# Kernel tuning notes

Hardware: AMD Instinct MI355X
Metric: run time of the kernel (lower is better)

Reference implementation:

```python
import jax, jax.numpy as jnp
import numpy as np

DIM = 256
NUM_HEADS = 8
HEAD_DIM = DIM // NUM_HEADS          # 32
KEY_DIM = int(HEAD_DIM * 0.5)        # 16
SCALE = KEY_DIM ** (-0.5)
QKV_OUT = DIM + 2 * KEY_DIM * NUM_HEADS  # 512
BN_EPS = 1e-3


def _bn(x, gamma, beta, mean, var):
    # inference-mode BatchNorm2d over channel axis 1 of NCHW
    inv = gamma / jnp.sqrt(var + BN_EPS)
    return x * inv[None, :, None, None] + (beta - mean * inv)[None, :, None, None]


def _conv1x1(x, w):
    # w: (O, C, 1, 1)
    return jnp.einsum('bchw,oc->bohw', x, w[:, :, 0, 0])


def _dwconv3x3(x, w):
    # depthwise 3x3, SAME padding; w: (C, 1, 3, 3)
    return jax.lax.conv_general_dilated(
        x, w, window_strides=(1, 1), padding='SAME',
        feature_group_count=x.shape[1],
        dimension_numbers=('NCHW', 'OIHW', 'NCHW'))


def setup_inputs() -> dict:
    key = jax.random.key(0)
    ks = jax.random.split(key, 16)
    B, C, H, W = 16, DIM, 32, 32
    inp = {
        'x': jax.random.normal(ks[0], (B, C, H, W), jnp.float32),
        'qkv_w': jax.random.normal(ks[1], (QKV_OUT, DIM, 1, 1), jnp.float32) * (1.0 / np.sqrt(DIM)),
        'qkv_gamma': jnp.ones((QKV_OUT,), jnp.float32),
        'qkv_beta': jnp.zeros((QKV_OUT,), jnp.float32),
        'qkv_mean': jax.random.normal(ks[2], (QKV_OUT,), jnp.float32) * 0.1,
        'qkv_var': jax.random.uniform(ks[3], (QKV_OUT,), jnp.float32, 0.5, 1.5),
        'pe_w': jax.random.normal(ks[4], (DIM, 1, 3, 3), jnp.float32) * (1.0 / 3.0),
        'pe_gamma': jnp.ones((DIM,), jnp.float32),
        'pe_beta': jnp.zeros((DIM,), jnp.float32),
        'pe_mean': jax.random.normal(ks[5], (DIM,), jnp.float32) * 0.1,
        'pe_var': jax.random.uniform(ks[6], (DIM,), jnp.float32, 0.5, 1.5),
        'proj_w': jax.random.normal(ks[7], (DIM, DIM, 1, 1), jnp.float32) * (1.0 / np.sqrt(DIM)),
        'proj_gamma': jnp.ones((DIM,), jnp.float32),
        'proj_beta': jnp.zeros((DIM,), jnp.float32),
        'proj_mean': jax.random.normal(ks[8], (DIM,), jnp.float32) * 0.1,
        'proj_var': jax.random.uniform(ks[9], (DIM,), jnp.float32, 0.5, 1.5),
    }
    return inp


def reference(x, qkv_w, qkv_gamma, qkv_beta, qkv_mean, qkv_var,
              pe_w, pe_gamma, pe_beta, pe_mean, pe_var,
              proj_w, proj_gamma, proj_beta, proj_mean, proj_var):
    B, C, H, W = x.shape
    N = H * W
    # qkv: 1x1 conv + BN (act=False)
    qkv = _bn(_conv1x1(x, qkv_w), qkv_gamma, qkv_beta, qkv_mean, qkv_var)
    qkv = qkv.reshape(B, NUM_HEADS, 2 * KEY_DIM + HEAD_DIM, N)
    q = qkv[:, :, :KEY_DIM]                          # (B, h, kd, N)
    k = qkv[:, :, KEY_DIM:2 * KEY_DIM]               # (B, h, kd, N)
    v = qkv[:, :, 2 * KEY_DIM:]                      # (B, h, hd, N)
    # attn = (q^T @ k) * scale, softmax over last dim
    attn = jnp.einsum('bhdn,bhdm->bhnm', q, k) * SCALE   # (B, h, N, N)
    attn = jax.nn.softmax(attn, axis=-1)
    # v @ attn^T
    v_attn = jnp.einsum('bhdn,bhmn->bhdm', v, attn)      # (B, h, hd, N)
    v_attn = v_attn.reshape(B, C, H, W)
    v_reshaped = v.reshape(B, C, H, W)
    pos_enc = _bn(_dwconv3x3(v_reshaped, pe_w), pe_gamma, pe_beta, pe_mean, pe_var)
    out = v_attn + pos_enc
    out = _bn(_conv1x1(out, proj_w), proj_gamma, proj_beta, proj_mean, proj_var)
    return out
```

## Files before the change

kernel.cpp:

```cpp
#include <hip/hip_runtime.h>

#define B_ 16
#define C_ 256
#define N_ 1024
#define NH 8
#define HD 32
#define KD 16
#define QKV_OUT_ 512
#define BN_EPS 1e-3f
#define SCALE2_ (0.25f * 1.44269504088896f)

typedef __attribute__((ext_vector_type(8))) short short8;
typedef __attribute__((ext_vector_type(16))) float float16;

__device__ inline unsigned short f2bf(float f) {
  unsigned int u = __float_as_uint(f);
  return (unsigned short)((u + 0x7FFF + ((u >> 16) & 1)) >> 16);
}
__device__ inline float bf2f(unsigned short s) {
  return __uint_as_float(((unsigned int)s) << 16);
}
__device__ inline float16 zero16() {
  float16 z;
  #pragma unroll
  for (int i = 0; i < 16; ++i) z[i] = 0.f;
  return z;
}
__device__ inline unsigned int pack_bf16_trunc(float a, float b) {
  return __builtin_amdgcn_perm(__float_as_uint(b), __float_as_uint(a), 0x07060302u);
}
__device__ inline unsigned int pack_bf16_rne(float a, float b) {
  return (unsigned int)f2bf(a) | ((unsigned int)f2bf(b) << 16);
}
__device__ inline float fast_exp2(float x) {
#if __has_builtin(__builtin_amdgcn_exp2f)
  return __builtin_amdgcn_exp2f(x);
#else
  return exp2f(x);
#endif
}
__device__ inline void pl32(unsigned int& a, unsigned int& b) {
#if __has_builtin(__builtin_amdgcn_permlane32_swap)
  typedef __attribute__((ext_vector_type(2))) int int2v;
  int2v r = __builtin_amdgcn_permlane32_swap((int)a, (int)b, false, false);
  a = (unsigned int)r[0];
  b = (unsigned int)r[1];
#else
  unsigned int ea = (unsigned int)__shfl_xor((int)a, 32, 64);
  unsigned int eb = (unsigned int)__shfl_xor((int)b, 32, 64);
  bool hi = (threadIdx.x & 32) != 0;
  unsigned int an = hi ? eb : a;
  unsigned int bn = hi ? b : ea;
  a = an; b = bn;
#endif
}
__device__ inline short8 lds_frag(const unsigned short* p) {
  union { uint2 u[2]; short8 s; } r;
  r.u[0] = *(const uint2*)p;
  r.u[1] = *(const uint2*)(p + 4);
  return r.s;
}
__device__ inline void lds_store16(unsigned short* p, uint4 v) {
  *(uint2*)p = make_uint2(v.x, v.y);
  *(uint2*)(p + 4) = make_uint2(v.z, v.w);
}

__global__ __launch_bounds__(256) void fold_weights(
    const float* __restrict__ qkv_w, const float* __restrict__ qg,
    const float* __restrict__ qb, const float* __restrict__ qm,
    const float* __restrict__ qv,
    const float* __restrict__ proj_w, const float* __restrict__ pg,
    const float* __restrict__ pb, const float* __restrict__ pm,
    const float* __restrict__ pv,
    unsigned short* __restrict__ wq, float* __restrict__ biasq,
    unsigned short* __restrict__ wp, float* __restrict__ biasp)
{
  const int o = blockIdx.x, c = threadIdx.x;
  if (o < QKV_OUT_) {
    float s = ((o & 63) < 16) ? SCALE2_ : 1.f;
    float inv = qg[o] * rsqrtf(qv[o] + BN_EPS) * s;
    wq[o * C_ + c] = f2bf(qkv_w[o * C_ + c] * inv);
    if (c == 0) biasq[o] = qb[o] * s - qm[o] * inv;
  } else {
    int oo = o - QKV_OUT_;
    float inv = pg[oo] * rsqrtf(pv[oo] + BN_EPS);
    wp[oo * C_ + c] = f2bf(proj_w[oo * C_ + c] * inv);
    if (c == 0) biasp[oo] = pb[oo] - pm[oo] * inv;
  }
}

__global__ __launch_bounds__(256) void transpose_x(
    const float* __restrict__ x, unsigned short* __restrict__ xT)
{
  __shared__ float t[64][69];
  const int tid = threadIdx.x;
  const int nt = blockIdx.x, ct = blockIdx.y, b = blockIdx.z;
  const int n0 = nt * 64, c0 = ct * 64;

  #pragma unroll
  for (int it = 0; it < 4; ++it) {
    int cl = it * 16 + (tid >> 4);
    int nl = (tid & 15) * 4;
    float4 v = *(const float4*)(x + ((size_t)b * C_ + c0 + cl) * N_ + n0 + nl);
    t[cl][nl + 0] = v.x; t[cl][nl + 1] = v.y;
    t[cl][nl + 2] = v.z; t[cl][nl + 3] = v.w;
  }
  __syncthreads();

  const int nr = tid >> 2, cseg = (tid & 3) * 16;
  unsigned int pk[8];
  #pragma unroll
  for (int q = 0; q < 8; ++q)
    pk[q] = pack_bf16_rne(t[cseg + 2 * q][nr], t[cseg + 2 * q + 1][nr]);
  unsigned short* row = xT + ((size_t)b * N_ + n0 + nr) * C_ + c0 + cseg;
  *(uint4*)(row)     = make_uint4(pk[0], pk[1], pk[2], pk[3]);
  *(uint4*)(row + 8) = make_uint4(pk[4], pk[5], pk[6], pk[7]);
}

template <int MODE>
__global__ __launch_bounds__(256) void gemm_tiled(
    const unsigned short* __restrict__ inT, const unsigned short* __restrict__ wfold,
    const float* __restrict__ bias,
    unsigned short* __restrict__ qkT, unsigned short* __restrict__ vbuf,
    float* __restrict__ outf)
{
  constexpr int STR = 44;
  __shared__ __align__(8) unsigned short wa[2][128 * STR];
  __shared__ __align__(8) unsigned short xb[2][128 * STR];
  const int tid = threadIdx.x;
  const int wave = tid >> 6, lane = tid & 63, l31 = lane & 31, lh = lane >> 5;
  const int wm = wave & 1, wn = wave >> 1;
  const int n0g = blockIdx.x * 128;
  const int o0 = blockIdx.y * 128;
  const int b = n0g >> 10, nloc = n0g & 1023;

  const int r0 = tid >> 2, oc0 = (tid & 3) * 8;
  const int r1 = (tid + 256) >> 2, oc1 = oc0;

  float16 acc[2][2];
  #pragma unroll
  for (int i = 0; i < 2; ++i)
    #pragma unroll
    for (int j = 0; j < 2; ++j) acc[i][j] = zero16();

  uint4 ga0, ga1, gb0, gb1;
  #define LOADK(kc)                                                          \
    ga0 = *(const uint4*)(wfold + (size_t)(o0 + r0) * C_ + (kc) * 32 + oc0); \
    ga1 = *(const uint4*)(wfold + (size_t)(o0 + r1) * C_ + (kc) * 32 + oc1); \
    gb0 = *(const uint4*)(inT + (size_t)(n0g + r0) * C_ + (kc) * 32 + oc0);  \
    gb1 = *(const uint4*)(inT + (size_t)(n0g + r1) * C_ + (kc) * 32 + oc1);
  #define STOREK(bufi)                                   \
    lds_store16(&wa[bufi][r0 * STR + oc0], ga0);         \
    lds_store16(&wa[bufi][r1 * STR + oc1], ga1);         \
    lds_store16(&xb[bufi][r0 * STR + oc0], gb0);         \
    lds_store16(&xb[bufi][r1 * STR + oc1], gb1);

  LOADK(0);
  STOREK(0);
  __syncthreads();

  for (int kc = 0; kc < 8; ++kc) {
    const int buf = kc & 1;
    if (kc < 7) { LOADK(kc + 1); }

    #pragma unroll
    for (int ks = 0; ks < 2; ++ks) {
      const int ko = ks * 16 + lh * 8;
      short8 a0 = lds_frag(&wa[buf][(wm * 64 + l31) * STR + ko]);
      short8 a1 = lds_frag(&wa[buf][(wm * 64 + 32 + l31) * STR + ko]);
      short8 b0 = lds_frag(&xb[buf][(wn * 64 + l31) * STR + ko]);
      short8 b1 = lds_frag(&xb[buf][(wn * 64 + 32 + l31) * STR + ko]);
      acc[0][0] = __builtin_amdgcn_mfma_f32_32x32x16_bf16(a0, b0, acc[0][0], 0, 0, 0);
      acc[0][1] = __builtin_amdgcn_mfma_f32_32x32x16_bf16(a0, b1, acc[0][1], 0, 0, 0);
      acc[1][0] = __builtin_amdgcn_mfma_f32_32x32x16_bf16(a1, b0, acc[1][0], 0, 0, 0);
      acc[1][1] = __builtin_amdgcn_mfma_f32_32x32x16_bf16(a1, b1, acc[1][1], 0, 0, 0);
    }

    if (kc < 7) { STOREK(buf ^ 1); }
    __syncthreads();
  }
  #undef LOADK
  #undef STOREK

  if constexpr (MODE == 0) {
    const int hh = (o0 >> 6) + wm;
    #pragma unroll
    for (int bn = 0; bn < 2; ++bn) {
      int n = nloc + wn * 64 + bn * 32 + l31;
      unsigned short* row = qkT + (((size_t)b * NH + hh) * N_ + n) * 32;
      #pragma unroll
      for (int qd = 0; qd < 4; ++qd) {
        int cc0 = 8 * qd + 4 * lh;
        ushort4 rv;
        rv.x = f2bf(acc[0][bn][4 * qd + 0] + bias[hh * 64 + cc0 + 0]);
        rv.y = f2bf(acc[0][bn][4 * qd + 1] + bias[hh * 64 + cc0 + 1]);
        rv.z = f2bf(acc[0][bn][4 * qd + 2] + bias[hh * 64 + cc0 + 2]);
        rv.w = f2bf(acc[0][bn][4 * qd + 3] + bias[hh * 64 + cc0 + 3]);
        *(ushort4*)(row + cc0) = rv;
      }
    }
    #pragma unroll
    for (int r = 0; r < 16; ++r) {
      int d = (r & 3) + 8 * (r >> 2) + 4 * lh;
      float bo = bias[hh * 64 + 32 + d];
      unsigned short* vrow =
          vbuf + ((size_t)b * C_ + hh * 32 + d) * N_ + nloc + wn * 64 + l31;
      #pragma unroll
      for (int bn = 0; bn < 2; ++bn)
        vrow[bn * 32] = f2bf(acc[1][bn][r] + bo);
    }
  } else {
    #pragma unroll
    for (int am = 0; am < 2; ++am) {
      #pragma unroll
      for (int r = 0; r < 16; ++r) {
        int o = o0 + wm * 64 + am * 32 + (r & 3) + 8 * (r >> 2) + 4 * lh;
        float bo = bias[o];
        float* orow = outf + ((size_t)b * C_ + o) * N_ + nloc + wn * 64 + l31;
        #pragma unroll
        for (int bn = 0; bn < 2; ++bn)
          orow[bn * 32] = acc[am][bn][r] + bo;
      }
    }
  }
}

__global__ __launch_bounds__(256) void dwconv_bn(
    const unsigned short* __restrict__ vbuf, const float* __restrict__ pw,
    const float* __restrict__ gamma, const float* __restrict__ beta,
    const float* __restrict__ mean, const float* __restrict__ var,
    unsigned short* __restrict__ posb)
{
  __shared__ float t[34][34];
  const int c = blockIdx.x, b = blockIdx.y;
  const int tid = threadIdx.x;
  const unsigned short* vp = vbuf + ((size_t)b * C_ + c) * N_;

  #pragma unroll
  for (int r = 0; r < 4; ++r) {
    int idx = r * 256 + tid;
    t[(idx >> 5) + 1][(idx & 31) + 1] = bf2f(vp[idx]);
  }
  if (tid < 34) {
    t[0][tid] = 0.f; t[33][tid] = 0.f;
    t[tid][0] = 0.f; t[tid][33] = 0.f;
  }
  __syncthreads();

  float w9[9];
  #pragma unroll
  for (int i = 0; i < 9; ++i) w9[i] = pw[c * 9 + i];
  float inv = gamma[c] * rsqrtf(var[c] + BN_EPS);
  float add = beta[c] - mean[c] * inv;

  unsigned short* op = posb + ((size_t)b * C_ + c) * N_;
  #pragma unroll
  for (int r = 0; r < 4; ++r) {
    int idx = r * 256 + tid;
    int y = idx >> 5, x = idx & 31;
    float s = 0.f;
    #pragma unroll
    for (int dy = 0; dy < 3; ++dy)
      #pragma unroll
      for (int dx = 0; dx < 3; ++dx)
        s += t[y + dy][x + dx] * w9[dy * 3 + dx];
    op[idx] = f2bf(s * inv + add);
  }
}

__global__ __launch_bounds__(256) void attn_mfma(
    const unsigned short* __restrict__ qkT, const unsigned short* __restrict__ vbuf,
    const unsigned short* __restrict__ posb, unsigned short* __restrict__ vattnT)
{
  __shared__ __align__(8) unsigned short k_lds[2][128 * 28];
  __shared__ __align__(8) unsigned short v_lds[2][32 * 140];

  const int tid = threadIdx.x;
  const int wave = tid >> 6, lane = tid & 63;
  const int l31 = lane & 31, lh = lane >> 5;
  const int h = blockIdx.y, b = blockIdx.z;
  const int qbase = blockIdx.x * 256 + wave * 64;

  const unsigned short* qkb = qkT + ((size_t)b * NH + h) * N_ * 32;
  const unsigned short* vhead = vbuf + ((size_t)b * C_ + h * HD) * N_;

  const int skey = tid >> 1, shalf = tid & 1;
  const int svd = tid >> 3, svseg = tid & 7;

  short8 qfA = lds_frag(qkb + (size_t)(qbase + l31) * 32 + lh * 8);
  short8 qfB = lds_frag(qkb + (size_t)(qbase + 32 + l31) * 32 + lh * 8);

  uint4 gk, gv0, gv1;
  #define LOADC(kc)                                                             \
    gk  = *(const uint4*)(qkb + (size_t)((kc) + skey) * 32 + 16 + shalf * 8);   \
    gv0 = *(const uint4*)(vhead + (size_t)svd * N_ + (kc) + svseg * 16);        \
    gv1 = *(const uint4*)(vhead + (size_t)svd * N_ + (kc) + svseg * 16 + 8);
  #define STOREC(bufi)                                        \
    lds_store16(&k_lds[bufi][skey * 28 + shalf * 8], gk);     \
    lds_store16(&v_lds[bufi][svd * 140 + svseg * 16], gv0);   \
    lds_store16(&v_lds[bufi][svd * 140 + svseg * 16 + 8], gv1);

  LOADC(0);
  STOREC(0);
  __syncthreads();

  float16 oaccA = zero16(), oaccB = zero16();
  float lsA[4] = {0.f, 0.f, 0.f, 0.f}, lsB[4] = {0.f, 0.f, 0.f, 0.f};

  for (int c = 0; c < 8; ++c) {
    const int buf = c & 1;
    if (c < 7) { LOADC((c + 1) * 128); }

    #pragma unroll
    for (int t = 0; t < 4; ++t) {
      const int key0 = t * 32;
      short8 kf = lds_frag(&k_lds[buf][(key0 + l31) * 28 + lh * 8]);
      float16 stA = __builtin_amdgcn_mfma_f32_32x32x16_bf16(kf, qfA, zero16(), 0, 0, 0);
      float16 stB = __builtin_amdgcn_mfma_f32_32x32x16_bf16(kf, qfB, zero16(), 0, 0, 0);

      unsigned int uA[8], uB[8];
      #pragma unroll
      for (int q = 0; q < 8; ++q) {
        float pe = fast_exp2(stA[2 * q]);
        float po = fast_exp2(stA[2 * q + 1]);
        lsA[q & 3] += pe + po;
        uA[q] = pack_bf16_trunc(pe, po);
      }
      #pragma unroll
      for (int q = 0; q < 8; ++q) {
        float pe = fast_exp2(stB[2 * q]);
        float po = fast_exp2(stB[2 * q + 1]);
        lsB[q & 3] += pe + po;
        uB[q] = pack_bf16_trunc(pe, po);
      }

      #pragma unroll
      for (int f = 0; f < 2; ++f) {
        short8 vf = lds_frag(&v_lds[buf][l31 * 140 + key0 + f * 16 + lh * 8]);
        const int q0 = f * 4;
        {
          unsigned int a0 = uA[q0], a2 = uA[q0 + 2]; pl32(a0, a2);
          unsigned int a1 = uA[q0 + 1], a3 = uA[q0 + 3]; pl32(a1, a3);
          union { unsigned int w[4]; short8 s; } bf;
          bf.w[0] = a0; bf.w[1] = a1; bf.w[2] = a2; bf.w[3] = a3;
          oaccA = __builtin_amdgcn_mfma_f32_32x32x16_bf16(vf, bf.s, oaccA, 0, 0, 0);
        }
        {
          unsigned int a0 = uB[q0], a2 = uB[q0 + 2]; pl32(a0, a2);
          unsigned int a1 = uB[q0 + 1], a3 = uB[q0 + 3]; pl32(a1, a3);
          union { unsigned int w[4]; short8 s; } bf;
          bf.w[0] = a0; bf.w[1] = a1; bf.w[2] = a2; bf.w[3] = a3;
          oaccB = __builtin_amdgcn_mfma_f32_32x32x16_bf16(vf, bf.s, oaccB, 0, 0, 0);
        }
      }
    }

    if (c < 7) { STOREC(buf ^ 1); }
    __syncthreads();
  }
  #undef LOADC
  #undef STOREC

  float lsumA = (lsA[0] + lsA[1]) + (lsA[2] + lsA[3]);
  float lsumB = (lsB[0] + lsB[1]) + (lsB[2] + lsB[3]);
  lsumA += __shfl_xor(lsumA, 32, 64);
  lsumB += __shfl_xor(lsumB, 32, 64);
  const float linvA = 1.f / lsumA, linvB = 1.f / lsumB;

  #pragma unroll
  for (int g = 0; g < 2; ++g) {
    const float16& oacc = g ? oaccB : oaccA;
    const float linv = g ? linvB : linvA;
    const int token = qbase + g * 32 + l31;
    float val[16];
    #pragma unroll
    for (int r = 0; r < 16; ++r) {
      int d = (r & 3) + 8 * (r >> 2) + 4 * lh;
      val[r] = oacc[r] * linv +
               bf2f(posb[((size_t)b * C_ + h * HD + d) * N_ + token]);
    }
    unsigned int u[8];
    #pragma unroll
    for (int m = 0; m < 8; ++m) u[m] = pack_bf16_rne(val[2 * m], val[2 * m + 1]);
    pl32(u[0], u[4]); pl32(u[1], u[5]); pl32(u[2], u[6]); pl32(u[3], u[7]);
    unsigned short* row = vattnT + ((size_t)b * N_ + token) * C_ + h * HD + lh * 16;
    *(uint4*)(row)     = make_uint4(u[0], u[1], u[4], u[5]);
    *(uint4*)(row + 8) = make_uint4(u[2], u[3], u[6], u[7]);
  }
}

extern "C" void kernel_launch(void* const* d_in, const int* in_sizes, int n_in,
                              void* d_out, int out_size, void* d_ws, size_t ws_size,
                              hipStream_t stream) {
  const float* x          = (const float*)d_in[0];
  const float* qkv_w      = (const float*)d_in[1];
  const float* qkv_gamma  = (const float*)d_in[2];
  const float* qkv_beta   = (const float*)d_in[3];
  const float* qkv_mean   = (const float*)d_in[4];
  const float* qkv_var    = (const float*)d_in[5];
  const float* pe_w       = (const float*)d_in[6];
  const float* pe_gamma   = (const float*)d_in[7];
  const float* pe_beta    = (const float*)d_in[8];
  const float* pe_mean    = (const float*)d_in[9];
  const float* pe_var     = (const float*)d_in[10];
  const float* proj_w     = (const float*)d_in[11];
  const float* proj_gamma = (const float*)d_in[12];
  const float* proj_beta  = (const float*)d_in[13];
  const float* proj_mean  = (const float*)d_in[14];
  const float* proj_var   = (const float*)d_in[15];
  float* out = (float*)d_out;

  char* ws = (char*)d_ws;
  unsigned short* qkT = (unsigned short*)ws;
  ws += (size_t)B_ * NH * N_ * 32 * sizeof(unsigned short);
  unsigned short* vbuf = (unsigned short*)ws;
  ws += (size_t)B_ * C_ * N_ * sizeof(unsigned short);
  unsigned short* xT = (unsigned short*)ws;
  ws += (size_t)B_ * N_ * C_ * sizeof(unsigned short);
  unsigned short* vattnT = (unsigned short*)ws;
  ws += (size_t)B_ * N_ * C_ * sizeof(unsigned short);
  unsigned short* posb = (unsigned short*)ws;
  ws += (size_t)B_ * C_ * N_ * sizeof(unsigned short);
  unsigned short* wq = (unsigned short*)ws;
  ws += (size_t)QKV_OUT_ * C_ * sizeof(unsigned short);
  unsigned short* wp = (unsigned short*)ws;
  ws += (size_t)C_ * C_ * sizeof(unsigned short);
  float* biasq = (float*)ws; ws += QKV_OUT_ * sizeof(float);
  float* biasp = (float*)ws;

  fold_weights<<<dim3(QKV_OUT_ + C_), 256, 0, stream>>>(
      qkv_w, qkv_gamma, qkv_beta, qkv_mean, qkv_var,
      proj_w, proj_gamma, proj_beta, proj_mean, proj_var,
      wq, biasq, wp, biasp);
  transpose_x<<<dim3(16, 4, 16), 256, 0, stream>>>(x, xT);

  gemm_tiled<0><<<dim3(128, 4), 256, 0, stream>>>(
      xT, wq, biasq, qkT, vbuf, nullptr);

  dwconv_bn<<<dim3(C_, B_), 256, 0, stream>>>(
      vbuf, pe_w, pe_gamma, pe_beta, pe_mean, pe_var, posb);

  attn_mfma<<<dim3(4, NH, B_), 256, 0, stream>>>(qkT, vbuf, posb, vattnT);

  gemm_tiled<1><<<dim3(128, 2), 256, 0, stream>>>(
      vattnT, wp, biasp, nullptr, nullptr, out);
}
```

Measured before the change: 161.3 us.

## Fuse x transpose into QKV GEMM and halve attention queries per block

Drops the separate transpose_x kernel. The QKV GEMM now reads fp32 x directly in NCHW, converts it to bf16 and writes it transposed into LDS, which removes one launch and the round trip of the xT buffer through global memory. The attention kernel gives each wave 32 queries instead of 64 and uses 128 queries per block, so the grid grows from 512 to 1024 blocks for more parallelism and fewer registers per wave. The cost is that each K/V tile is loaded into LDS twice as often, and the strided per-element global loads of x in the GEMM may coalesce less well.

```diff
diff --git a/kernel.cpp b/kernel.cpp
--- a/kernel.cpp
+++ b/kernel.cpp
@@ -89,40 +89,10 @@
   }
 }
 
-__global__ __launch_bounds__(256) void transpose_x(
-    const float* __restrict__ x, unsigned short* __restrict__ xT)
-{
-  __shared__ float t[64][69];
-  const int tid = threadIdx.x;
-  const int nt = blockIdx.x, ct = blockIdx.y, b = blockIdx.z;
-  const int n0 = nt * 64, c0 = ct * 64;
-
-  #pragma unroll
-  for (int it = 0; it < 4; ++it) {
-    int cl = it * 16 + (tid >> 4);
-    int nl = (tid & 15) * 4;
-    float4 v = *(const float4*)(x + ((size_t)b * C_ + c0 + cl) * N_ + n0 + nl);
-    t[cl][nl + 0] = v.x; t[cl][nl + 1] = v.y;
-    t[cl][nl + 2] = v.z; t[cl][nl + 3] = v.w;
-  }
-  __syncthreads();
-
-  const int nr = tid >> 2, cseg = (tid & 3) * 16;
-  unsigned int pk[8];
-  #pragma unroll
-  for (int q = 0; q < 8; ++q)
-    pk[q] = pack_bf16_rne(t[cseg + 2 * q][nr], t[cseg + 2 * q + 1][nr]);
-  unsigned short* row = xT + ((size_t)b * N_ + n0 + nr) * C_ + c0 + cseg;
-  *(uint4*)(row)     = make_uint4(pk[0], pk[1], pk[2], pk[3]);
-  *(uint4*)(row + 8) = make_uint4(pk[4], pk[5], pk[6], pk[7]);
-}
-
-template <int MODE>
-__global__ __launch_bounds__(256) void gemm_tiled(
-    const unsigned short* __restrict__ inT, const unsigned short* __restrict__ wfold,
+__global__ __launch_bounds__(256) void gemm_qkv(
+    const float* __restrict__ x, const unsigned short* __restrict__ wq,
     const float* __restrict__ bias,
-    unsigned short* __restrict__ qkT, unsigned short* __restrict__ vbuf,
-    float* __restrict__ outf)
+    unsigned short* __restrict__ qkT, unsigned short* __restrict__ vbuf)
 {
   constexpr int STR = 44;
   __shared__ __align__(8) unsigned short wa[2][128 * STR];
@@ -130,12 +100,33 @@
   const int tid = threadIdx.x;
   const int wave = tid >> 6, lane = tid & 63, l31 = lane & 31, lh = lane >> 5;
   const int wm = wave & 1, wn = wave >> 1;
-  const int n0g = blockIdx.x * 128;
+  const int b = blockIdx.x >> 3, nloc = (blockIdx.x & 7) * 128;
   const int o0 = blockIdx.y * 128;
-  const int b = n0g >> 10, nloc = n0g & 1023;
 
   const int r0 = tid >> 2, oc0 = (tid & 3) * 8;
-  const int r1 = (tid + 256) >> 2, oc1 = oc0;
+  const int r1 = r0 + 64;
+  const int tok = tid & 127, chalf = (tid >> 7) * 16;
+  const float* xbase = x + (size_t)b * C_ * N_ + nloc + tok;
+
+  uint4 ga0, ga1;
+  float nb[16];
+
+  auto loadk = [&](int kc) {
+    ga0 = *(const uint4*)(wq + (size_t)(o0 + r0) * C_ + kc * 32 + oc0);
+    ga1 = *(const uint4*)(wq + (size_t)(o0 + r1) * C_ + kc * 32 + oc0);
+    #pragma unroll
+    for (int j = 0; j < 16; ++j)
+      nb[j] = xbase[(size_t)(kc * 32 + chalf + j) * N_];
+  };
+  auto storek = [&](int bufi) {
+    lds_store16(&wa[bufi][r0 * STR + oc0], ga0);
+    lds_store16(&wa[bufi][r1 * STR + oc0], ga1);
+    unsigned int pk[8];
+    #pragma unroll
+    for (int q = 0; q < 8; ++q) pk[q] = pack_bf16_rne(nb[2 * q], nb[2 * q + 1]);
+    lds_store16(&xb[bufi][tok * STR + chalf], make_uint4(pk[0], pk[1], pk[2], pk[3]));
+    lds_store16(&xb[bufi][tok * STR + chalf + 8], make_uint4(pk[4], pk[5], pk[6], pk[7]));
+  };
 
   float16 acc[2][2];
   #pragma unroll
@@ -143,25 +134,13 @@
     #pragma unroll
     for (int j = 0; j < 2; ++j) acc[i][j] = zero16();
 
-  uint4 ga0, ga1, gb0, gb1;
-  #define LOADK(kc)                                                          \
-    ga0 = *(const uint4*)(wfold + (size_t)(o0 + r0) * C_ + (kc) * 32 + oc0); \
-    ga1 = *(const uint4*)(wfold + (size_t)(o0 + r1) * C_ + (kc) * 32 + oc1); \
-    gb0 = *(const uint4*)(inT + (size_t)(n0g + r0) * C_ + (kc) * 32 + oc0);  \
-    gb1 = *(const uint4*)(inT + (size_t)(n0g + r1) * C_ + (kc) * 32 + oc1);
-  #define STOREK(bufi)                                   \
-    lds_store16(&wa[bufi][r0 * STR + oc0], ga0);         \
-    lds_store16(&wa[bufi][r1 * STR + oc1], ga1);         \
-    lds_store16(&xb[bufi][r0 * STR + oc0], gb0);         \
-    lds_store16(&xb[bufi][r1 * STR + oc1], gb1);
-
-  LOADK(0);
-  STOREK(0);
+  loadk(0);
+  storek(0);
   __syncthreads();
 
   for (int kc = 0; kc < 8; ++kc) {
     const int buf = kc & 1;
-    if (kc < 7) { LOADK(kc + 1); }
+    if (kc < 7) loadk(kc + 1);
 
     #pragma unroll
     for (int ks = 0; ks < 2; ++ks) {
@@ -176,51 +155,110 @@
       acc[1][1] = __builtin_amdgcn_mfma_f32_32x32x16_bf16(a1, b1, acc[1][1], 0, 0, 0);
     }
 
-    if (kc < 7) { STOREK(buf ^ 1); }
+    if (kc < 7) storek(buf ^ 1);
     __syncthreads();
   }
-  #undef LOADK
-  #undef STOREK
-
-  if constexpr (MODE == 0) {
-    const int hh = (o0 >> 6) + wm;
-    #pragma unroll
-    for (int bn = 0; bn < 2; ++bn) {
-      int n = nloc + wn * 64 + bn * 32 + l31;
-      unsigned short* row = qkT + (((size_t)b * NH + hh) * N_ + n) * 32;
-      #pragma unroll
-      for (int qd = 0; qd < 4; ++qd) {
-        int cc0 = 8 * qd + 4 * lh;
-        ushort4 rv;
-        rv.x = f2bf(acc[0][bn][4 * qd + 0] + bias[hh * 64 + cc0 + 0]);
-        rv.y = f2bf(acc[0][bn][4 * qd + 1] + bias[hh * 64 + cc0 + 1]);
-        rv.z = f2bf(acc[0][bn][4 * qd + 2] + bias[hh * 64 + cc0 + 2]);
-        rv.w = f2bf(acc[0][bn][4 * qd + 3] + bias[hh * 64 + cc0 + 3]);
-        *(ushort4*)(row + cc0) = rv;
-      }
+
+  const int hh = (o0 >> 6) + wm;
+  #pragma unroll
+  for (int bn = 0; bn < 2; ++bn) {
+    int n = nloc + wn * 64 + bn * 32 + l31;
+    unsigned short* row = qkT + (((size_t)b * NH + hh) * N_ + n) * 32;
+    #pragma unroll
+    for (int qd = 0; qd < 4; ++qd) {
+      int cc0 = 8 * qd + 4 * lh;
+      ushort4 rv;
+      rv.x = f2bf(acc[0][bn][4 * qd + 0] + bias[hh * 64 + cc0 + 0]);
+      rv.y = f2bf(acc[0][bn][4 * qd + 1] + bias[hh * 64 + cc0 + 1]);
+      rv.z = f2bf(acc[0][bn][4 * qd + 2] + bias[hh * 64 + cc0 + 2]);
+      rv.w = f2bf(acc[0][bn][4 * qd + 3] + bias[hh * 64 + cc0 + 3]);
+      *(ushort4*)(row + cc0) = rv;
     }
+  }
+  #pragma unroll
+  for (int r = 0; r < 16; ++r) {
+    int d = (r & 3) + 8 * (r >> 2) + 4 * lh;
+    float bo = bias[hh * 64 + 32 + d];
+    unsigned short* vrow =
+        vbuf + ((size_t)b * C_ + hh * 32 + d) * N_ + nloc + wn * 64 + l31;
+    #pragma unroll
+    for (int bn = 0; bn < 2; ++bn)
+      vrow[bn * 32] = f2bf(acc[1][bn][r] + bo);
+  }
+}
+
+__global__ __launch_bounds__(256) void gemm_proj(
+    const unsigned short* __restrict__ inT, const unsigned short* __restrict__ wfold,
+    const float* __restrict__ bias, float* __restrict__ outf)
+{
+  constexpr int STR = 44;
+  __shared__ __align__(8) unsigned short wa[2][128 * STR];
+  __shared__ __align__(8) unsigned short xb[2][128 * STR];
+  const int tid = threadIdx.x;
+  const int wave = tid >> 6, lane = tid & 63, l31 = lane & 31, lh = lane >> 5;
+  const int wm = wave & 1, wn = wave >> 1;
+  const int n0g = blockIdx.x * 128;
+  const int o0 = blockIdx.y * 128;
+  const int b = n0g >> 10, nloc = n0g & 1023;
+
+  const int r0 = tid >> 2, oc0 = (tid & 3) * 8;
+  const int r1 = r0 + 64;
+
+  float16 acc[2][2];
+  #pragma unroll
+  for (int i = 0; i < 2; ++i)
+    #pragma unroll
+    for (int j = 0; j < 2; ++j) acc[i][j] = zero16();
+
+  uint4 ga0, ga1, gb0, gb1;
+  auto loadk = [&](int kc) {
+    ga0 = *(const uint4*)(wfold + (size_t)(o0 + r0) * C_ + kc * 32 + oc0);
+    ga1 = *(const uint4*)(wfold + (size_t)(o0 + r1) * C_ + kc * 32 + oc0);
+    gb0 = *(const uint4*)(inT + (size_t)(n0g + r0) * C_ + kc * 32 + oc0);
+    gb1 = *(const uint4*)(inT + (size_t)(n0g + r1) * C_ + kc * 32 + oc0);
+  };
+  auto storek = [&](int bufi) {
+    lds_store16(&wa[bufi][r0 * STR + oc0], ga0);
+    lds_store16(&wa[bufi][r1 * STR + oc0], ga1);
+    lds_store16(&xb[bufi][r0 * STR + oc0], gb0);
+    lds_store16(&xb[bufi][r1 * STR + oc0], gb1);
+  };
+
+  loadk(0);
+  storek(0);
+  __syncthreads();
+
+  for (int kc = 0; kc < 8; ++kc) {
+    const int buf = kc & 1;
+    if (kc < 7) loadk(kc + 1);
+
+    #pragma unroll
+    for (int ks = 0; ks < 2; ++ks) {
+      const int ko = ks * 16 + lh * 8;
+      short8 a0 = lds_frag(&wa[buf][(wm * 64 + l31) * STR + ko]);
+      short8 a1 = lds_frag(&wa[buf][(wm * 64 + 32 + l31) * STR + ko]);
+      short8 b0 = lds_frag(&xb[buf][(wn * 64 + l31) * STR + ko]);
+      short8 b1 = lds_frag(&xb[buf][(wn * 64 + 32 + l31) * STR + ko]);
+      acc[0][0] = __builtin_amdgcn_mfma_f32_32x32x16_bf16(a0, b0, acc[0][0], 0, 0, 0);
+      acc[0][1] = __builtin_amdgcn_mfma_f32_32x32x16_bf16(a0, b1, acc[0][1], 0, 0, 0);
+      acc[1][0] = __builtin_amdgcn_mfma_f32_32x32x16_bf16(a1, b0, acc[1][0], 0, 0, 0);
+      acc[1][1] = __builtin_amdgcn_mfma_f32_32x32x16_bf16(a1, b1, acc[1][1], 0, 0, 0);
+    }
+
+    if (kc < 7) storek(buf ^ 1);
+    __syncthreads();
+  }
+
+  #pragma unroll
+  for (int am = 0; am < 2; ++am) {
     #pragma unroll
     for (int r = 0; r < 16; ++r) {
-      int d = (r & 3) + 8 * (r >> 2) + 4 * lh;
-      float bo = bias[hh * 64 + 32 + d];
-      unsigned short* vrow =
-          vbuf + ((size_t)b * C_ + hh * 32 + d) * N_ + nloc + wn * 64 + l31;
+      int o = o0 + wm * 64 + am * 32 + (r & 3) + 8 * (r >> 2) + 4 * lh;
+      float bo = bias[o];
+      float* orow = outf + ((size_t)b * C_ + o) * N_ + nloc + wn * 64 + l31;
       #pragma unroll
       for (int bn = 0; bn < 2; ++bn)
-        vrow[bn * 32] = f2bf(acc[1][bn][r] + bo);
-    }
-  } else {
-    #pragma unroll
-    for (int am = 0; am < 2; ++am) {
-      #pragma unroll
-      for (int r = 0; r < 16; ++r) {
-        int o = o0 + wm * 64 + am * 32 + (r & 3) + 8 * (r >> 2) + 4 * lh;
-        float bo = bias[o];
-        float* orow = outf + ((size_t)b * C_ + o) * N_ + nloc + wn * 64 + l31;
-        #pragma unroll
-        for (int bn = 0; bn < 2; ++bn)
-          orow[bn * 32] = acc[am][bn][r] + bo;
-      }
+        orow[bn * 32] = acc[am][bn][r] + bo;
     }
   }
 }
@@ -278,8 +316,8 @@
   const int tid = threadIdx.x;
   const int wave = tid >> 6, lane = tid & 63;
   const int l31 = lane & 31, lh = lane >> 5;
-  const int h = blockIdx.y, b = blockIdx.z;
-  const int qbase = blockIdx.x * 256 + wave * 64;
+  const int b = blockIdx.x >> 3, h = blockIdx.x & 7;
+  const int qbase = blockIdx.y * 128 + wave * 32;
 
   const unsigned short* qkb = qkT + ((size_t)b * NH + h) * N_ * 32;
   const unsigned short* vhead = vbuf + ((size_t)b * C_ + h * HD) * N_;
@@ -287,106 +325,81 @@
   const int skey = tid >> 1, shalf = tid & 1;
   const int svd = tid >> 3, svseg = tid & 7;
 
-  short8 qfA = lds_frag(qkb + (size_t)(qbase + l31) * 32 + lh * 8);
-  short8 qfB = lds_frag(qkb + (size_t)(qbase + 32 + l31) * 32 + lh * 8);
+  short8 qf = lds_frag(qkb + (size_t)(qbase + l31) * 32 + lh * 8);
 
   uint4 gk, gv0, gv1;
-  #define LOADC(kc)                                                             \
-    gk  = *(const uint4*)(qkb + (size_t)((kc) + skey) * 32 + 16 + shalf * 8);   \
-    gv0 = *(const uint4*)(vhead + (size_t)svd * N_ + (kc) + svseg * 16);        \
-    gv1 = *(const uint4*)(vhead + (size_t)svd * N_ + (kc) + svseg * 16 + 8);
-  #define STOREC(bufi)                                        \
-    lds_store16(&k_lds[bufi][skey * 28 + shalf * 8], gk);     \
-    lds_store16(&v_lds[bufi][svd * 140 + svseg * 16], gv0);   \
+  auto loadc = [&](int kc) {
+    gk  = *(const uint4*)(qkb + (size_t)(kc + skey) * 32 + 16 + shalf * 8);
+    gv0 = *(const uint4*)(vhead + (size_t)svd * N_ + kc + svseg * 16);
+    gv1 = *(const uint4*)(vhead + (size_t)svd * N_ + kc + svseg * 16 + 8);
+  };
+  auto storec = [&](int bufi) {
+    lds_store16(&k_lds[bufi][skey * 28 + shalf * 8], gk);
+    lds_store16(&v_lds[bufi][svd * 140 + svseg * 16], gv0);
     lds_store16(&v_lds[bufi][svd * 140 + svseg * 16 + 8], gv1);
-
-  LOADC(0);
-  STOREC(0);
+  };
+
+  loadc(0);
+  storec(0);
   __syncthreads();
 
-  float16 oaccA = zero16(), oaccB = zero16();
-  float lsA[4] = {0.f, 0.f, 0.f, 0.f}, lsB[4] = {0.f, 0.f, 0.f, 0.f};
+  float16 oacc = zero16();
+  float ls[4] = {0.f, 0.f, 0.f, 0.f};
 
   for (int c = 0; c < 8; ++c) {
     const int buf = c & 1;
-    if (c < 7) { LOADC((c + 1) * 128); }
+    if (c < 7) loadc((c + 1) * 128);
 
     #pragma unroll
     for (int t = 0; t < 4; ++t) {
       const int key0 = t * 32;
       short8 kf = lds_frag(&k_lds[buf][(key0 + l31) * 28 + lh * 8]);
-      float16 stA = __builtin_amdgcn_mfma_f32_32x32x16_bf16(kf, qfA, zero16(), 0, 0, 0);
-      float16 stB = __builtin_amdgcn_mfma_f32_32x32x16_bf16(kf, qfB, zero16(), 0, 0, 0);
-
-      unsigned int uA[8], uB[8];
+      float16 st = __builtin_amdgcn_mfma_f32_32x32x16_bf16(kf, qf, zero16(), 0, 0, 0);
+
+      unsigned int u[8];
       #pragma unroll
       for (int q = 0; q < 8; ++q) {
-        float pe = fast_exp2(stA[2 * q]);
-        float po = fast_exp2(stA[2 * q + 1]);
-        lsA[q & 3] += pe + po;
-        uA[q] = pack_bf16_trunc(pe, po);
-      }
-      #pragma unroll
-      for (int q = 0; q < 8; ++q) {
-        float pe = fast_exp2(stB[2 * q]);
-        float po = fast_exp2(stB[2 * q + 1]);
-        lsB[q & 3] += pe + po;
-        uB[q] = pack_bf16_trunc(pe, po);
+        float pe = fast_exp2(st[2 * q]);
+        float po = fast_exp2(st[2 * q + 1]);
+        ls[q & 3] += pe + po;
+        u[q] = pack_bf16_trunc(pe, po);
       }
 
       #pragma unroll
       for (int f = 0; f < 2; ++f) {
         short8 vf = lds_frag(&v_lds[buf][l31 * 140 + key0 + f * 16 + lh * 8]);
         const int q0 = f * 4;
-        {
-          unsigned int a0 = uA[q0], a2 = uA[q0 + 2]; pl32(a0, a2);
-          unsigned int a1 = uA[q0 + 1], a3 = uA[q0 + 3]; pl32(a1, a3);
-          union { unsigned int w[4]; short8 s; } bf;
-          bf.w[0] = a0; bf.w[1] = a1; bf.w[2] = a2; bf.w[3] = a3;
-          oaccA = __builtin_amdgcn_mfma_f32_32x32x16_bf16(vf, bf.s, oaccA, 0, 0, 0);
-        }
-        {
-          unsigned int a0 = uB[q0], a2 = uB[q0 + 2]; pl32(a0, a2);
-          unsigned int a1 = uB[q0 + 1], a3 = uB[q0 + 3]; pl32(a1, a3);
-          union { unsigned int w[4]; short8 s; } bf;
-          bf.w[0] = a0; bf.w[1] = a1; bf.w[2] = a2; bf.w[3] = a3;
-          oaccB = __builtin_amdgcn_mfma_f32_32x32x16_bf16(vf, bf.s, oaccB, 0, 0, 0);
-        }
+        unsigned int a0 = u[q0], a2 = u[q0 + 2]; pl32(a0, a2);
+        unsigned int a1 = u[q0 + 1], a3 = u[q0 + 3]; pl32(a1, a3);
+        union { unsigned int w[4]; short8 s; } bf;
+        bf.w[0] = a0; bf.w[1] = a1; bf.w[2] = a2; bf.w[3] = a3;
+        oacc = __builtin_amdgcn_mfma_f32_32x32x16_bf16(vf, bf.s, oacc, 0, 0, 0);
       }
     }
 
-    if (c < 7) { STOREC(buf ^ 1); }
+    if (c < 7) storec(buf ^ 1);
     __syncthreads();
   }
-  #undef LOADC
-  #undef STOREC
-
-  float lsumA = (lsA[0] + lsA[1]) + (lsA[2] + lsA[3]);
-  float lsumB = (lsB[0] + lsB[1]) + (lsB[2] + lsB[3]);
-  lsumA += __shfl_xor(lsumA, 32, 64);
-  lsumB += __shfl_xor(lsumB, 32, 64);
-  const float linvA = 1.f / lsumA, linvB = 1.f / lsumB;
-
-  #pragma unroll
-  for (int g = 0; g < 2; ++g) {
-    const float16& oacc = g ? oaccB : oaccA;
-    const float linv = g ? linvB : linvA;
-    const int token = qbase + g * 32 + l31;
-    float val[16];
-    #pragma unroll
-    for (int r = 0; r < 16; ++r) {
-      int d = (r & 3) + 8 * (r >> 2) + 4 * lh;
-      val[r] = oacc[r] * linv +
-               bf2f(posb[((size_t)b * C_ + h * HD + d) * N_ + token]);
-    }
-    unsigned int u[8];
-    #pragma unroll
-    for (int m = 0; m < 8; ++m) u[m] = pack_bf16_rne(val[2 * m], val[2 * m + 1]);
-    pl32(u[0], u[4]); pl32(u[1], u[5]); pl32(u[2], u[6]); pl32(u[3], u[7]);
-    unsigned short* row = vattnT + ((size_t)b * N_ + token) * C_ + h * HD + lh * 16;
-    *(uint4*)(row)     = make_uint4(u[0], u[1], u[4], u[5]);
-    *(uint4*)(row + 8) = make_uint4(u[2], u[3], u[6], u[7]);
-  }
+
+  float lsum = (ls[0] + ls[1]) + (ls[2] + ls[3]);
+  lsum += __shfl_xor(lsum, 32, 64);
+  const float linv = 1.f / lsum;
+
+  const int token = qbase + l31;
+  float val[16];
+  #pragma unroll
+  for (int r = 0; r < 16; ++r) {
+    int d = (r & 3) + 8 * (r >> 2) + 4 * lh;
+    val[r] = oacc[r] * linv +
+             bf2f(posb[((size_t)b * C_ + h * HD + d) * N_ + token]);
+  }
+  unsigned int u[8];
+  #pragma unroll
+  for (int m = 0; m < 8; ++m) u[m] = pack_bf16_rne(val[2 * m], val[2 * m + 1]);
+  pl32(u[0], u[4]); pl32(u[1], u[5]); pl32(u[2], u[6]); pl32(u[3], u[7]);
+  unsigned short* row = vattnT + ((size_t)b * N_ + token) * C_ + h * HD + lh * 16;
+  *(uint4*)(row)     = make_uint4(u[0], u[1], u[4], u[5]);
+  *(uint4*)(row + 8) = make_uint4(u[2], u[3], u[6], u[7]);
 }
 
 extern "C" void kernel_launch(void* const* d_in, const int* in_sizes, int n_in,
@@ -415,8 +428,6 @@
   ws += (size_t)B_ * NH * N_ * 32 * sizeof(unsigned short);
   unsigned short* vbuf = (unsigned short*)ws;
   ws += (size_t)B_ * C_ * N_ * sizeof(unsigned short);
-  unsigned short* xT = (unsigned short*)ws;
-  ws += (size_t)B_ * N_ * C_ * sizeof(unsigned short);
   unsigned short* vattnT = (unsigned short*)ws;
   ws += (size_t)B_ * N_ * C_ * sizeof(unsigned short);
   unsigned short* posb = (unsigned short*)ws;
@@ -432,16 +443,13 @@
       qkv_w, qkv_gamma, qkv_beta, qkv_mean, qkv_var,
       proj_w, proj_gamma, proj_beta, proj_mean, proj_var,
       wq, biasq, wp, biasp);
-  transpose_x<<<dim3(16, 4, 16), 256, 0, stream>>>(x, xT);
-
-  gemm_tiled<0><<<dim3(128, 4), 256, 0, stream>>>(
-      xT, wq, biasq, qkT, vbuf, nullptr);
+
+  gemm_qkv<<<dim3(128, 4), 256, 0, stream>>>(x, wq, biasq, qkT, vbuf);
 
   dwconv_bn<<<dim3(C_, B_), 256, 0, stream>>>(
       vbuf, pe_w, pe_gamma, pe_beta, pe_mean, pe_var, posb);
 
-  attn_mfma<<<dim3(4, NH, B_), 256, 0, stream>>>(qkT, vbuf, posb, vattnT);
-
-  gemm_tiled<1><<<dim3(128, 2), 256, 0, stream>>>(
-      vattnT, wp, biasp, nullptr, nullptr, out);
-}
+  attn_mfma<<<dim3(128, 8), 256, 0, stream>>>(qkT, vbuf, posb, vattnT);
+
+  gemm_proj<<<dim3(128, 2), 256, 0, stream>>>(vattnT, wp, biasp, out);
+}
```

After: 156.5 us. 3.0% less time.
